# Kernel optimization log

Hardware: AMD Instinct MI355X
Metric: run time of the kernel (lower is better)

## Reference

```python
import jax, jax.numpy as jnp
import numpy as np

B, T, C, H = 8, 4096, 1024, 64

def setup_inputs() -> dict:
    key = jax.random.key(0)
    k1, k2, k3, k4 = jax.random.split(key, 4)
    return {
        "x": jax.random.normal(k1, (B, T, C), dtype=jnp.float32),
        "Wq": jax.random.normal(k2, (C, H), dtype=jnp.float32) * (C ** -0.5),
        "Wk": jax.random.normal(k3, (C, H), dtype=jnp.float32) * (C ** -0.5),
        "Wv": jax.random.normal(k4, (C, H), dtype=jnp.float32) * (C ** -0.5),
    }

def reference(x, Wq, Wk, Wv):
    # x: [B, T, C]; projections are bias-free Linears
    q = jnp.einsum("btc,ch->bth", x, Wq)  # [B, T, H]
    k = jnp.einsum("btc,ch->bth", x, Wk)
    v = jnp.einsum("btc,ch->bth", x, Wv)
    # NOTE: original scales by C**-0.5 (embed size), not head_size**-0.5
    scores = jnp.einsum("bqh,bkh->bqk", q, k) * (x.shape[-1] ** -0.5)  # [B, T, T]
    causal = jnp.tril(jnp.ones((x.shape[1], x.shape[1]), dtype=bool))
    scores = jnp.where(causal, scores, -jnp.inf)
    weights = jax.nn.softmax(scores, axis=-1)
    # dropout p=0.0 (eval) -> identity
    return jnp.einsum("bqk,bkh->bqh", weights, v)  # [B, T, H]
```

## Files before the change

kernel.cpp:

```cpp
#include <hip/hip_runtime.h>
#include <hip/hip_bf16.h>

typedef __attribute__((ext_vector_type(8))) short short8;
typedef __attribute__((ext_vector_type(4))) float f32x4;
typedef unsigned short u16;
typedef unsigned int u32;
typedef unsigned long long u64;

typedef u64    __attribute__((may_alias)) u64a;
typedef short8 __attribute__((may_alias)) short8a;
typedef float4 __attribute__((may_alias)) float4a;

#define Tseq 4096
#define LPP  72

__device__ __forceinline__ u32 pk_bf(float a, float b) {
    union { __hip_bfloat162 h; u32 u; } t;
    float2 f; f.x = a; f.y = b;
    t.h = __float22bfloat162_rn(f);
    return t.u;
}

__device__ __forceinline__ u16 f2bf(float f) {
    u32 u = __float_as_uint(f);
    u = (u + 0x7FFFu + ((u >> 16) & 1u)) >> 16;
    return (u16)u;
}

__device__ __forceinline__ short8 ld_frag_lds(const u16* p) {
    union { short8 v; u64 u[2]; } t;
    t.u[0] = *(const u64a*)(p);
    t.u[1] = *(const u64a*)(p + 4);
    return t.v;
}

__device__ __forceinline__ short8 cvt8(float4 a, float4 b) {
    union { short8 s; u32 u[4]; } t;
    t.u[0] = pk_bf(a.x, a.y); t.u[1] = pk_bf(a.z, a.w);
    t.u[2] = pk_bf(b.x, b.y); t.u[3] = pk_bf(b.z, b.w);
    return t.s;
}

__device__ __forceinline__ void gld_lds16(const void* g, void* l) {
    __builtin_amdgcn_global_load_lds(
        (const __attribute__((address_space(1))) u32*)g,
        (__attribute__((address_space(3))) u32*)l, 16, 0, 0);
}

__global__ __launch_bounds__(256) void wt_kernel(const float* __restrict__ Wq,
                                                 const float* __restrict__ Wk,
                                                 const float* __restrict__ Wv,
                                                 u16* __restrict__ wtf) {
    int idx = blockIdx.x * 256 + threadIdx.x;
    int lane = idx & 63, cc = (idx >> 6) & 31, n = (idx >> 11) & 3, mat = idx >> 13;
    const float* W = (mat == 0) ? Wq : ((mat == 1) ? Wk : Wv);
    float sc = (mat == 0) ? 0.03125f : 1.0f;
    int h = n * 16 + (lane & 15);
    int cbase = cc * 32 + (lane >> 4) * 8;
    union { short8 s; u32 u[4]; } t;
#pragma unroll
    for (int j2 = 0; j2 < 4; ++j2) {
        float a = W[(size_t)(cbase + j2 * 2)     * 64 + h] * sc;
        float b = W[(size_t)(cbase + j2 * 2 + 1) * 64 + h] * sc;
        t.u[j2] = pk_bf(a, b);
    }
    *(short8a*)(wtf + (size_t)idx * 8) = t.s;
}

__global__ __launch_bounds__(256, 2) void proj_kernel(const float* __restrict__ x,
                                                      const u16* __restrict__ wtf,
                                                      u16* __restrict__ qb,
                                                      u16* __restrict__ kA,
                                                      u16* __restrict__ vA) {
    __shared__ __align__(16) u16 Wl[2][12 * 2 * 64 * 8];

    const int tid = threadIdx.x, lane = tid & 63, wave = tid >> 6;
    const int m = lane & 15, quad = lane >> 4;
    const long rowbase = (long)blockIdx.x * 64 + wave * 16;
    const float* xr = x + (rowbase + m) * 1024 + quad * 8;

    f32x4 acc[12];
#pragma unroll
    for (int i = 0; i < 12; ++i) acc[i] = (f32x4){0.f, 0.f, 0.f, 0.f};

#define STAGE(p, buf)                                                          \
    {                                                                          \
        _Pragma("unroll")                                                      \
        for (int i = 0; i < 6; ++i) {                                          \
            int c = wave * 6 + i, mn = c >> 1, ccp = c & 1;                    \
            const u16* g = wtf + ((size_t)(mn * 32 + (p) * 2 + ccp) * 64 + lane) * 8; \
            u16* l = &Wl[buf][(size_t)(mn * 2 + ccp) * 512];                   \
            gld_lds16(g, l);                                                   \
        }                                                                      \
    }

    float4 xa[4], xb[4];
#pragma unroll
    for (int t = 0; t < 4; ++t)
        xa[t] = *(const float4a*)(xr + (t >> 1) * 32 + (t & 1) * 4);
#pragma unroll
    for (int t = 0; t < 4; ++t)
        xb[t] = *(const float4a*)(xr + (2 + (t >> 1)) * 32 + (t & 1) * 4);

    STAGE(0, 0);
    __syncthreads();

    for (int p = 0; p < 16; ++p) {
        if (p < 15) STAGE(p + 1, (p + 1) & 1);
        float4 xn[4];
        if (p < 14) {
#pragma unroll
            for (int t = 0; t < 4; ++t)
                xn[t] = *(const float4a*)(xr + (2 * (p + 2) + (t >> 1)) * 32 + (t & 1) * 4);
        }
        const u16* wb = Wl[p & 1];
#pragma unroll
        for (int ccp = 0; ccp < 2; ++ccp) {
            short8 af = cvt8(xa[ccp * 2], xa[ccp * 2 + 1]);
#pragma unroll
            for (int mn = 0; mn < 12; ++mn) {
                short8 bf = *(const short8a*)(wb + ((size_t)(mn * 2 + ccp) * 64 + lane) * 8);
                acc[mn] = __builtin_amdgcn_mfma_f32_16x16x32_bf16(af, bf, acc[mn], 0, 0, 0);
            }
        }
#pragma unroll
        for (int t = 0; t < 4; ++t) { xa[t] = xb[t]; if (p < 14) xb[t] = xn[t]; }
        __syncthreads();
    }
#undef STAGE

    const int b  = (int)(rowbase >> 12);
    const int tb = (int)(rowbase & 4095);

#pragma unroll
    for (int n = 0; n < 4; ++n)
#pragma unroll
        for (int r = 0; r < 4; ++r)
            qb[(rowbase + quad * 4 + r) * 64 + n * 16 + m] = f2bf(acc[n][r]);

#pragma unroll
    for (int n = 0; n < 4; ++n) {
        int kk = n >> 1;
        int lq = (n * 2 + (m >> 3)) & 3;
        int j  = m & 7;
#pragma unroll
        for (int r = 0; r < 4; ++r) {
            int key = tb + quad * 4 + r;
            size_t a = ((((size_t)b * 256 + (key >> 4)) * 2 + kk) * 64
                        + ((key & 15) + 16 * lq)) * 8 + j;
            kA[a] = f2bf(acc[4 + n][r]);
        }
    }

    {
        int key0 = tb + quad * 4;
        int j0 = key0 & 7;
        int q2 = (key0 >> 3) & 3;
        int kc = key0 >> 5;
#pragma unroll
        for (int n = 0; n < 4; ++n) {
            u64 pv = (u64)pk_bf(acc[8 + n][0], acc[8 + n][1])
                   | ((u64)pk_bf(acc[8 + n][2], acc[8 + n][3]) << 32);
            size_t a = ((((size_t)b * 4 + n) * 128 + kc) * 64 + (m + 16 * q2)) * 8 + j0;
            *(u64a*)(vA + a) = pv;
        }
    }
}

struct K8 { short8 k[8]; };

__device__ __forceinline__ void loadK(K8& f, const u16* kAb, int kt, int lane) {
    const u16* kp = kAb + (size_t)kt * 4096 + (size_t)lane * 8;
#pragma unroll
    for (int mt = 0; mt < 4; ++mt) {
        f.k[mt * 2]     = *(const short8a*)(kp + mt * 1024);
        f.k[mt * 2 + 1] = *(const short8a*)(kp + mt * 1024 + 512);
    }
}

__device__ __forceinline__ void attn_step(const K8& f, const u16* vAb,
        short8 qf0, short8 qf1, u16* pw,
        f32x4& o0, f32x4& o1, f32x4& o2, f32x4& o3,
        float& lsum, int kt, int n_s, int qrow, int quad, int m, int lane) {
    const float L2E = 1.4426950408889634f;
    const float FMB = 4.0f * L2E;
    const u16* vp = vAb + (size_t)kt * 1024 + (size_t)lane * 8;
    short8 vf[8];
#pragma unroll
    for (int ht = 0; ht < 4; ++ht) {
        vf[ht * 2]     = *(const short8a*)(vp + (size_t)ht * 65536);
        vf[ht * 2 + 1] = *(const short8a*)(vp + (size_t)ht * 65536 + 512);
    }
    f32x4 s[4];
#pragma unroll
    for (int mt = 0; mt < 4; ++mt) {
        f32x4 a = (f32x4){0.f, 0.f, 0.f, 0.f};
        a = __builtin_amdgcn_mfma_f32_16x16x32_bf16(f.k[mt * 2],     qf0, a, 0, 0, 0);
        a = __builtin_amdgcn_mfma_f32_16x16x32_bf16(f.k[mt * 2 + 1], qf1, a, 0, 0, 0);
        s[mt] = a;
    }
    if (kt == n_s) {
#pragma unroll
        for (int mt = 0; mt < 4; ++mt)
#pragma unroll
            for (int r = 0; r < 4; ++r) {
                int key = kt * 64 + mt * 16 + quad * 4 + r;
                if (key > qrow) s[mt][r] = -1e30f;
            }
    }
#pragma unroll
    for (int mt = 0; mt < 4; ++mt) {
        float p0 = __builtin_amdgcn_exp2f(s[mt][0] * L2E - FMB);
        float p1 = __builtin_amdgcn_exp2f(s[mt][1] * L2E - FMB);
        float p2 = __builtin_amdgcn_exp2f(s[mt][2] * L2E - FMB);
        float p3 = __builtin_amdgcn_exp2f(s[mt][3] * L2E - FMB);
        lsum += (p0 + p1) + (p2 + p3);
        u64 pv = (u64)pk_bf(p0, p1) | ((u64)pk_bf(p2, p3) << 32);
        *(u64a*)(pw + m * LPP + mt * 16 + quad * 4) = pv;
    }
    __builtin_amdgcn_wave_barrier();
    short8 pf0 = ld_frag_lds(pw + m * LPP + quad * 8);
    short8 pf1 = ld_frag_lds(pw + m * LPP + 32 + quad * 8);
    o0 = __builtin_amdgcn_mfma_f32_16x16x32_bf16(vf[0], pf0, o0, 0, 0, 0);
    o0 = __builtin_amdgcn_mfma_f32_16x16x32_bf16(vf[1], pf1, o0, 0, 0, 0);
    o1 = __builtin_amdgcn_mfma_f32_16x16x32_bf16(vf[2], pf0, o1, 0, 0, 0);
    o1 = __builtin_amdgcn_mfma_f32_16x16x32_bf16(vf[3], pf1, o1, 0, 0, 0);
    o2 = __builtin_amdgcn_mfma_f32_16x16x32_bf16(vf[4], pf0, o2, 0, 0, 0);
    o2 = __builtin_amdgcn_mfma_f32_16x16x32_bf16(vf[5], pf1, o2, 0, 0, 0);
    o3 = __builtin_amdgcn_mfma_f32_16x16x32_bf16(vf[6], pf0, o3, 0, 0, 0);
    o3 = __builtin_amdgcn_mfma_f32_16x16x32_bf16(vf[7], pf1, o3, 0, 0, 0);
}

__global__ __launch_bounds__(256, 3) void attn_kernel(const u16* __restrict__ qb,
                                                      const u16* __restrict__ kA,
                                                      const u16* __restrict__ vA,
                                                      float* __restrict__ out) {
    __shared__ __align__(16) u16 Pt[4][16 * LPP];
    __shared__ float Ob[2][16][64];
    __shared__ float Lb[2][64];

    const int tid = threadIdx.x, lane = tid & 63, wave = tid >> 6;
    const int m = lane & 15, quad = lane >> 4;
    const int beta = blockIdx.x;
    const int b = beta & 7, u = beta >> 3;
    const int role = (wave + beta) & 3;
    const int slot = role >> 1;
    const int half = role & 1;
    const int s = slot ? (255 - u) : u;
    const int qbase = s * 16;
    const int n_s = s >> 2;
    const int h = (n_s + 1) >> 1;
    const int kt0 = half ? h : 0;
    const int kt1 = half ? n_s : (h - 1);

    const u16* qp = qb + ((size_t)b * Tseq + qbase + m) * 64;
    short8 qf0 = *(const short8a*)(qp + quad * 8);
    short8 qf1 = *(const short8a*)(qp + 32 + quad * 8);

    const u16* kAb = kA + (size_t)b * (256 * 2 * 64 * 8);
    const u16* vAb = vA + (size_t)b * (4 * 128 * 64 * 8);
    u16* pw = Pt[wave];

    f32x4 o0 = {0.f, 0.f, 0.f, 0.f}, o1 = o0, o2 = o0, o3 = o0;
    float lsum = 0.f;
    const int qrow = qbase + m;

    if (kt0 <= kt1) {
        K8 ka, kb2;
        loadK(ka, kAb, kt0, lane);
        int kt = kt0;
        while (true) {
            if (kt < kt1) loadK(kb2, kAb, kt + 1, lane);
            attn_step(ka, vAb, qf0, qf1, pw, o0, o1, o2, o3, lsum,
                      kt, n_s, qrow, quad, m, lane);
            if (kt == kt1) break;
            ++kt;
            if (kt < kt1) loadK(ka, kAb, kt + 1, lane);
            attn_step(kb2, vAb, qf0, qf1, pw, o0, o1, o2, o3, lsum,
                      kt, n_s, qrow, quad, m, lane);
            if (kt == kt1) break;
            ++kt;
        }
    }

    if (half == 1) {
#pragma unroll
        for (int hn = 0; hn < 4; ++hn) {
            Ob[slot][hn * 4 + 0][lane] = o0[hn];
        }
        Ob[slot][0][lane] = o0[0]; Ob[slot][1][lane] = o0[1];
        Ob[slot][2][lane] = o0[2]; Ob[slot][3][lane] = o0[3];
        Ob[slot][4][lane] = o1[0]; Ob[slot][5][lane] = o1[1];
        Ob[slot][6][lane] = o1[2]; Ob[slot][7][lane] = o1[3];
        Ob[slot][8][lane] = o2[0]; Ob[slot][9][lane] = o2[1];
        Ob[slot][10][lane] = o2[2]; Ob[slot][11][lane] = o2[3];
        Ob[slot][12][lane] = o3[0]; Ob[slot][13][lane] = o3[1];
        Ob[slot][14][lane] = o3[2]; Ob[slot][15][lane] = o3[3];
        Lb[slot][lane] = lsum;
    }
    __syncthreads();
    if (half == 0) {
        o0[0] += Ob[slot][0][lane]; o0[1] += Ob[slot][1][lane];
        o0[2] += Ob[slot][2][lane]; o0[3] += Ob[slot][3][lane];
        o1[0] += Ob[slot][4][lane]; o1[1] += Ob[slot][5][lane];
        o1[2] += Ob[slot][6][lane]; o1[3] += Ob[slot][7][lane];
        o2[0] += Ob[slot][8][lane]; o2[1] += Ob[slot][9][lane];
        o2[2] += Ob[slot][10][lane]; o2[3] += Ob[slot][11][lane];
        o3[0] += Ob[slot][12][lane]; o3[1] += Ob[slot][13][lane];
        o3[2] += Ob[slot][14][lane]; o3[3] += Ob[slot][15][lane];
        lsum += Lb[slot][lane];

        lsum += __shfl_xor(lsum, 16, 64);
        lsum += __shfl_xor(lsum, 32, 64);
        float inv = 1.0f / lsum;

        float* orow = out + ((size_t)b * Tseq + qbase + m) * 64;
        float4 w;
        w.x = o0[0] * inv; w.y = o0[1] * inv; w.z = o0[2] * inv; w.w = o0[3] * inv;
        *(float4a*)(orow + 0 * 16 + quad * 4) = w;
        w.x = o1[0] * inv; w.y = o1[1] * inv; w.z = o1[2] * inv; w.w = o1[3] * inv;
        *(float4a*)(orow + 1 * 16 + quad * 4) = w;
        w.x = o2[0] * inv; w.y = o2[1] * inv; w.z = o2[2] * inv; w.w = o2[3] * inv;
        *(float4a*)(orow + 2 * 16 + quad * 4) = w;
        w.x = o3[0] * inv; w.y = o3[1] * inv; w.z = o3[2] * inv; w.w = o3[3] * inv;
        *(float4a*)(orow + 3 * 16 + quad * 4) = w;
    }
}

extern "C" void kernel_launch(void* const* d_in, const int* in_sizes, int n_in,
                              void* d_out, int out_size, void* d_ws, size_t ws_size,
                              hipStream_t stream) {
    const float* x  = (const float*)d_in[0];
    const float* Wq = (const float*)d_in[1];
    const float* Wk = (const float*)d_in[2];
    const float* Wv = (const float*)d_in[3];
    float* out = (float*)d_out;

    char* ws = (char*)d_ws;
    u16* wtf = (u16*)ws;
    u16* qb  = (u16*)(ws + 512 * 1024);
    u16* kA  = (u16*)(ws + 512 * 1024 + 4 * 1024 * 1024);
    u16* vA  = (u16*)(ws + 512 * 1024 + 8 * 1024 * 1024);

    wt_kernel<<<96, 256, 0, stream>>>(Wq, Wk, Wv, wtf);
    proj_kernel<<<512, 256, 0, stream>>>(x, wtf, qb, kA, vA);
    attn_kernel<<<1024, 256, 0, stream>>>(qb, kA, vA, out);
}
```

Before: 253.2 us.

## Balance causal key-tile work across waves with adaptive 1/3 or 2/2 strip split

Each block processes a short and a long causal query strip. Before, each strip got exactly two waves splitting its key tiles in half. Now the kernel computes, per block, whether giving the short strip one wave and the long strip three waves, or two and two, gives the smaller maximum per-wave tile count. Key tiles are then partitioned evenly among that strip's waves. Partial outputs and row sums are reduced through a larger shared buffer. The aim is to cut the slowest wave's work per block, at the cost of more LDS and a short reduction loop.

```diff
diff --git a/kernel.cpp b/kernel.cpp
--- a/kernel.cpp
+++ b/kernel.cpp
@@ -236,22 +236,32 @@
                                                       const u16* __restrict__ vA,
                                                       float* __restrict__ out) {
     __shared__ __align__(16) u16 Pt[4][16 * LPP];
-    __shared__ float Ob[2][16][64];
-    __shared__ float Lb[2][64];
+    __shared__ float Ob[4][16][64];
+    __shared__ float Lb[4][64];
 
     const int tid = threadIdx.x, lane = tid & 63, wave = tid >> 6;
     const int m = lane & 15, quad = lane >> 4;
     const int beta = blockIdx.x;
     const int b = beta & 7, u = beta >> 3;
-    const int role = (wave + beta) & 3;
-    const int slot = role >> 1;
-    const int half = role & 1;
-    const int s = slot ? (255 - u) : u;
+
+    const int T0 = (u >> 2) + 1;
+    const int T1 = 64 - (u >> 2);
+    const int max13 = (T0 > (T1 + 2) / 3) ? T0 : (T1 + 2) / 3;
+    const int c22a = (T0 + 1) >> 1, c22b = (T1 + 1) >> 1;
+    const int max22 = (c22a > c22b) ? c22a : c22b;
+    const int n0 = (max13 <= max22) ? 1 : 2;
+    const int n1 = 4 - n0;
+
+    const int r = (wave + beta) & 3;
+    const int strip_id = (r < n0) ? 0 : 1;
+    const int part   = strip_id ? (r - n0) : r;
+    const int nparts = strip_id ? n1 : n0;
+    const int T      = strip_id ? T1 : T0;
+    const int s      = strip_id ? (255 - u) : u;
     const int qbase = s * 16;
     const int n_s = s >> 2;
-    const int h = (n_s + 1) >> 1;
-    const int kt0 = half ? h : 0;
-    const int kt1 = half ? n_s : (h - 1);
+    const int kt0 = part * T / nparts;
+    const int kt1 = (part + 1) * T / nparts - 1;
 
     const u16* qp = qb + ((size_t)b * Tseq + qbase + m) * 64;
     short8 qf0 = *(const short8a*)(qp + quad * 8);
@@ -283,32 +293,32 @@
         }
     }
 
-    if (half == 1) {
-#pragma unroll
-        for (int hn = 0; hn < 4; ++hn) {
-            Ob[slot][hn * 4 + 0][lane] = o0[hn];
-        }
-        Ob[slot][0][lane] = o0[0]; Ob[slot][1][lane] = o0[1];
-        Ob[slot][2][lane] = o0[2]; Ob[slot][3][lane] = o0[3];
-        Ob[slot][4][lane] = o1[0]; Ob[slot][5][lane] = o1[1];
-        Ob[slot][6][lane] = o1[2]; Ob[slot][7][lane] = o1[3];
-        Ob[slot][8][lane] = o2[0]; Ob[slot][9][lane] = o2[1];
-        Ob[slot][10][lane] = o2[2]; Ob[slot][11][lane] = o2[3];
-        Ob[slot][12][lane] = o3[0]; Ob[slot][13][lane] = o3[1];
-        Ob[slot][14][lane] = o3[2]; Ob[slot][15][lane] = o3[3];
-        Lb[slot][lane] = lsum;
+    if (part != 0) {
+        Ob[r][0][lane] = o0[0]; Ob[r][1][lane] = o0[1];
+        Ob[r][2][lane] = o0[2]; Ob[r][3][lane] = o0[3];
+        Ob[r][4][lane] = o1[0]; Ob[r][5][lane] = o1[1];
+        Ob[r][6][lane] = o1[2]; Ob[r][7][lane] = o1[3];
+        Ob[r][8][lane] = o2[0]; Ob[r][9][lane] = o2[1];
+        Ob[r][10][lane] = o2[2]; Ob[r][11][lane] = o2[3];
+        Ob[r][12][lane] = o3[0]; Ob[r][13][lane] = o3[1];
+        Ob[r][14][lane] = o3[2]; Ob[r][15][lane] = o3[3];
+        Lb[r][lane] = lsum;
     }
     __syncthreads();
-    if (half == 0) {
-        o0[0] += Ob[slot][0][lane]; o0[1] += Ob[slot][1][lane];
-        o0[2] += Ob[slot][2][lane]; o0[3] += Ob[slot][3][lane];
-        o1[0] += Ob[slot][4][lane]; o1[1] += Ob[slot][5][lane];
-        o1[2] += Ob[slot][6][lane]; o1[3] += Ob[slot][7][lane];
-        o2[0] += Ob[slot][8][lane]; o2[1] += Ob[slot][9][lane];
-        o2[2] += Ob[slot][10][lane]; o2[3] += Ob[slot][11][lane];
-        o3[0] += Ob[slot][12][lane]; o3[1] += Ob[slot][13][lane];
-        o3[2] += Ob[slot][14][lane]; o3[3] += Ob[slot][15][lane];
-        lsum += Lb[slot][lane];
+    if (part == 0) {
+#pragma unroll 1
+        for (int pr = 1; pr < nparts; ++pr) {
+            const int rr = r + pr;
+            o0[0] += Ob[rr][0][lane]; o0[1] += Ob[rr][1][lane];
+            o0[2] += Ob[rr][2][lane]; o0[3] += Ob[rr][3][lane];
+            o1[0] += Ob[rr][4][lane]; o1[1] += Ob[rr][5][lane];
+            o1[2] += Ob[rr][6][lane]; o1[3] += Ob[rr][7][lane];
+            o2[0] += Ob[rr][8][lane]; o2[1] += Ob[rr][9][lane];
+            o2[2] += Ob[rr][10][lane]; o2[3] += Ob[rr][11][lane];
+            o3[0] += Ob[rr][12][lane]; o3[1] += Ob[rr][13][lane];
+            o3[2] += Ob[rr][14][lane]; o3[3] += Ob[rr][15][lane];
+            lsum += Lb[rr][lane];
+        }
 
         lsum += __shfl_xor(lsum, 16, 64);
         lsum += __shfl_xor(lsum, 32, 64);
```

After: 252.3 us. About the same (-0.4%).

## Share K/V tiles across four query waves via double-buffered LDS staging

Applied to the files above, without the earlier changes.

The attention kernel changes from each wave streaming its own K/V fragments from global memory (with a two-wave split-KV and an LDS reduction) to each block handling 64 consecutive query rows. The four waves cooperatively load each 64-key K/V tile into double-buffered shared memory with gld_lds16, and every wave reads it from there. The aim is to cut redundant global/L2 traffic for K and V and to drop the split-KV combine step. In exchange there is a block-wide barrier per key tile, more LDS use, lower occupancy (launch bounds 2, 512 blocks), and coarser causal load balance.

```diff
diff --git a/kernel.cpp b/kernel.cpp
--- a/kernel.cpp
+++ b/kernel.cpp
@@ -167,91 +167,22 @@
     }
 }
 
-struct K8 { short8 k[8]; };
-
-__device__ __forceinline__ void loadK(K8& f, const u16* kAb, int kt, int lane) {
-    const u16* kp = kAb + (size_t)kt * 4096 + (size_t)lane * 8;
-#pragma unroll
-    for (int mt = 0; mt < 4; ++mt) {
-        f.k[mt * 2]     = *(const short8a*)(kp + mt * 1024);
-        f.k[mt * 2 + 1] = *(const short8a*)(kp + mt * 1024 + 512);
-    }
-}
-
-__device__ __forceinline__ void attn_step(const K8& f, const u16* vAb,
-        short8 qf0, short8 qf1, u16* pw,
-        f32x4& o0, f32x4& o1, f32x4& o2, f32x4& o3,
-        float& lsum, int kt, int n_s, int qrow, int quad, int m, int lane) {
-    const float L2E = 1.4426950408889634f;
-    const float FMB = 4.0f * L2E;
-    const u16* vp = vAb + (size_t)kt * 1024 + (size_t)lane * 8;
-    short8 vf[8];
-#pragma unroll
-    for (int ht = 0; ht < 4; ++ht) {
-        vf[ht * 2]     = *(const short8a*)(vp + (size_t)ht * 65536);
-        vf[ht * 2 + 1] = *(const short8a*)(vp + (size_t)ht * 65536 + 512);
-    }
-    f32x4 s[4];
-#pragma unroll
-    for (int mt = 0; mt < 4; ++mt) {
-        f32x4 a = (f32x4){0.f, 0.f, 0.f, 0.f};
-        a = __builtin_amdgcn_mfma_f32_16x16x32_bf16(f.k[mt * 2],     qf0, a, 0, 0, 0);
-        a = __builtin_amdgcn_mfma_f32_16x16x32_bf16(f.k[mt * 2 + 1], qf1, a, 0, 0, 0);
-        s[mt] = a;
-    }
-    if (kt == n_s) {
-#pragma unroll
-        for (int mt = 0; mt < 4; ++mt)
-#pragma unroll
-            for (int r = 0; r < 4; ++r) {
-                int key = kt * 64 + mt * 16 + quad * 4 + r;
-                if (key > qrow) s[mt][r] = -1e30f;
-            }
-    }
-#pragma unroll
-    for (int mt = 0; mt < 4; ++mt) {
-        float p0 = __builtin_amdgcn_exp2f(s[mt][0] * L2E - FMB);
-        float p1 = __builtin_amdgcn_exp2f(s[mt][1] * L2E - FMB);
-        float p2 = __builtin_amdgcn_exp2f(s[mt][2] * L2E - FMB);
-        float p3 = __builtin_amdgcn_exp2f(s[mt][3] * L2E - FMB);
-        lsum += (p0 + p1) + (p2 + p3);
-        u64 pv = (u64)pk_bf(p0, p1) | ((u64)pk_bf(p2, p3) << 32);
-        *(u64a*)(pw + m * LPP + mt * 16 + quad * 4) = pv;
-    }
-    __builtin_amdgcn_wave_barrier();
-    short8 pf0 = ld_frag_lds(pw + m * LPP + quad * 8);
-    short8 pf1 = ld_frag_lds(pw + m * LPP + 32 + quad * 8);
-    o0 = __builtin_amdgcn_mfma_f32_16x16x32_bf16(vf[0], pf0, o0, 0, 0, 0);
-    o0 = __builtin_amdgcn_mfma_f32_16x16x32_bf16(vf[1], pf1, o0, 0, 0, 0);
-    o1 = __builtin_amdgcn_mfma_f32_16x16x32_bf16(vf[2], pf0, o1, 0, 0, 0);
-    o1 = __builtin_amdgcn_mfma_f32_16x16x32_bf16(vf[3], pf1, o1, 0, 0, 0);
-    o2 = __builtin_amdgcn_mfma_f32_16x16x32_bf16(vf[4], pf0, o2, 0, 0, 0);
-    o2 = __builtin_amdgcn_mfma_f32_16x16x32_bf16(vf[5], pf1, o2, 0, 0, 0);
-    o3 = __builtin_amdgcn_mfma_f32_16x16x32_bf16(vf[6], pf0, o3, 0, 0, 0);
-    o3 = __builtin_amdgcn_mfma_f32_16x16x32_bf16(vf[7], pf1, o3, 0, 0, 0);
-}
-
-__global__ __launch_bounds__(256, 3) void attn_kernel(const u16* __restrict__ qb,
+__global__ __launch_bounds__(256, 2) void attn_kernel(const u16* __restrict__ qb,
                                                       const u16* __restrict__ kA,
                                                       const u16* __restrict__ vA,
                                                       float* __restrict__ out) {
+    __shared__ __align__(16) u16 KVl[2][2][4096];
     __shared__ __align__(16) u16 Pt[4][16 * LPP];
-    __shared__ float Ob[2][16][64];
-    __shared__ float Lb[2][64];
 
     const int tid = threadIdx.x, lane = tid & 63, wave = tid >> 6;
     const int m = lane & 15, quad = lane >> 4;
     const int beta = blockIdx.x;
-    const int b = beta & 7, u = beta >> 3;
-    const int role = (wave + beta) & 3;
-    const int slot = role >> 1;
-    const int half = role & 1;
-    const int s = slot ? (255 - u) : u;
-    const int qbase = s * 16;
-    const int n_s = s >> 2;
-    const int h = (n_s + 1) >> 1;
-    const int kt0 = half ? h : 0;
-    const int kt1 = half ? n_s : (h - 1);
+    const int b = beta & 7;
+    const int u = beta >> 3;
+    const int g = (u < 32) ? (63 - u) : (u - 32);
+
+    const int qbase = (g * 4 + wave) * 16;
+    const int qrow = qbase + m;
 
     const u16* qp = qb + ((size_t)b * Tseq + qbase + m) * 64;
     short8 qf0 = *(const short8a*)(qp + quad * 8);
@@ -263,68 +194,109 @@
 
     f32x4 o0 = {0.f, 0.f, 0.f, 0.f}, o1 = o0, o2 = o0, o3 = o0;
     float lsum = 0.f;
-    const int qrow = qbase + m;
-
-    if (kt0 <= kt1) {
-        K8 ka, kb2;
-        loadK(ka, kAb, kt0, lane);
-        int kt = kt0;
-        while (true) {
-            if (kt < kt1) loadK(kb2, kAb, kt + 1, lane);
-            attn_step(ka, vAb, qf0, qf1, pw, o0, o1, o2, o3, lsum,
-                      kt, n_s, qrow, quad, m, lane);
-            if (kt == kt1) break;
-            ++kt;
-            if (kt < kt1) loadK(ka, kAb, kt + 1, lane);
-            attn_step(kb2, vAb, qf0, qf1, pw, o0, o1, o2, o3, lsum,
-                      kt, n_s, qrow, quad, m, lane);
-            if (kt == kt1) break;
-            ++kt;
-        }
-    }
-
-    if (half == 1) {
-#pragma unroll
-        for (int hn = 0; hn < 4; ++hn) {
-            Ob[slot][hn * 4 + 0][lane] = o0[hn];
-        }
-        Ob[slot][0][lane] = o0[0]; Ob[slot][1][lane] = o0[1];
-        Ob[slot][2][lane] = o0[2]; Ob[slot][3][lane] = o0[3];
-        Ob[slot][4][lane] = o1[0]; Ob[slot][5][lane] = o1[1];
-        Ob[slot][6][lane] = o1[2]; Ob[slot][7][lane] = o1[3];
-        Ob[slot][8][lane] = o2[0]; Ob[slot][9][lane] = o2[1];
-        Ob[slot][10][lane] = o2[2]; Ob[slot][11][lane] = o2[3];
-        Ob[slot][12][lane] = o3[0]; Ob[slot][13][lane] = o3[1];
-        Ob[slot][14][lane] = o3[2]; Ob[slot][15][lane] = o3[3];
-        Lb[slot][lane] = lsum;
-    }
+
+    const float L2E = 1.4426950408889634f;
+    const float FMB = 4.0f * L2E;
+
+#define ASTAGE(kt, bf)                                                         \
+    {                                                                          \
+        if (wave < 2) {                                                        \
+            _Pragma("unroll")                                                  \
+            for (int i = 0; i < 4; ++i) {                                      \
+                int c = wave * 4 + i;                                          \
+                const u16* gp = kAb + (size_t)(kt) * 4096 + c * 512 + lane * 8;\
+                gld_lds16(gp, &KVl[bf][0][c * 512]);                           \
+            }                                                                  \
+        } else {                                                               \
+            _Pragma("unroll")                                                  \
+            for (int i = 0; i < 4; ++i) {                                      \
+                int j = (wave - 2) * 4 + i, ht = j >> 1, hf = j & 1;           \
+                const u16* gp = vAb + (size_t)(kt) * 1024 + (size_t)ht * 65536 \
+                                + hf * 512 + lane * 8;                         \
+                gld_lds16(gp, &KVl[bf][1][ht * 1024 + hf * 512]);              \
+            }                                                                  \
+        }                                                                      \
+    }
+
+    ASTAGE(0, 0);
     __syncthreads();
-    if (half == 0) {
-        o0[0] += Ob[slot][0][lane]; o0[1] += Ob[slot][1][lane];
-        o0[2] += Ob[slot][2][lane]; o0[3] += Ob[slot][3][lane];
-        o1[0] += Ob[slot][4][lane]; o1[1] += Ob[slot][5][lane];
-        o1[2] += Ob[slot][6][lane]; o1[3] += Ob[slot][7][lane];
-        o2[0] += Ob[slot][8][lane]; o2[1] += Ob[slot][9][lane];
-        o2[2] += Ob[slot][10][lane]; o2[3] += Ob[slot][11][lane];
-        o3[0] += Ob[slot][12][lane]; o3[1] += Ob[slot][13][lane];
-        o3[2] += Ob[slot][14][lane]; o3[3] += Ob[slot][15][lane];
-        lsum += Lb[slot][lane];
-
-        lsum += __shfl_xor(lsum, 16, 64);
-        lsum += __shfl_xor(lsum, 32, 64);
-        float inv = 1.0f / lsum;
-
-        float* orow = out + ((size_t)b * Tseq + qbase + m) * 64;
-        float4 w;
-        w.x = o0[0] * inv; w.y = o0[1] * inv; w.z = o0[2] * inv; w.w = o0[3] * inv;
-        *(float4a*)(orow + 0 * 16 + quad * 4) = w;
-        w.x = o1[0] * inv; w.y = o1[1] * inv; w.z = o1[2] * inv; w.w = o1[3] * inv;
-        *(float4a*)(orow + 1 * 16 + quad * 4) = w;
-        w.x = o2[0] * inv; w.y = o2[1] * inv; w.z = o2[2] * inv; w.w = o2[3] * inv;
-        *(float4a*)(orow + 2 * 16 + quad * 4) = w;
-        w.x = o3[0] * inv; w.y = o3[1] * inv; w.z = o3[2] * inv; w.w = o3[3] * inv;
-        *(float4a*)(orow + 3 * 16 + quad * 4) = w;
-    }
+
+    int buf = 0;
+    for (int kt = 0; kt <= g; ++kt) {
+        if (kt < g) ASTAGE(kt + 1, buf ^ 1);
+
+        const u16* Klb = KVl[buf][0];
+        const u16* Vlb = KVl[buf][1];
+
+        short8 vf[8];
+#pragma unroll
+        for (int ht = 0; ht < 4; ++ht) {
+            vf[ht * 2]     = *(const short8a*)(Vlb + ht * 1024 + lane * 8);
+            vf[ht * 2 + 1] = *(const short8a*)(Vlb + ht * 1024 + 512 + lane * 8);
+        }
+
+        f32x4 s[4];
+#pragma unroll
+        for (int mt = 0; mt < 4; ++mt) {
+            short8 kf0 = *(const short8a*)(Klb + mt * 1024 + lane * 8);
+            short8 kf1 = *(const short8a*)(Klb + mt * 1024 + 512 + lane * 8);
+            f32x4 a = (f32x4){0.f, 0.f, 0.f, 0.f};
+            a = __builtin_amdgcn_mfma_f32_16x16x32_bf16(kf0, qf0, a, 0, 0, 0);
+            a = __builtin_amdgcn_mfma_f32_16x16x32_bf16(kf1, qf1, a, 0, 0, 0);
+            s[mt] = a;
+        }
+
+        if (kt == g) {
+#pragma unroll
+            for (int mt = 0; mt < 4; ++mt)
+#pragma unroll
+                for (int r = 0; r < 4; ++r) {
+                    int key = kt * 64 + mt * 16 + quad * 4 + r;
+                    if (key > qrow) s[mt][r] = -1e30f;
+                }
+        }
+
+#pragma unroll
+        for (int mt = 0; mt < 4; ++mt) {
+            float p0 = __builtin_amdgcn_exp2f(s[mt][0] * L2E - FMB);
+            float p1 = __builtin_amdgcn_exp2f(s[mt][1] * L2E - FMB);
+            float p2 = __builtin_amdgcn_exp2f(s[mt][2] * L2E - FMB);
+            float p3 = __builtin_amdgcn_exp2f(s[mt][3] * L2E - FMB);
+            lsum += (p0 + p1) + (p2 + p3);
+            u64 pv = (u64)pk_bf(p0, p1) | ((u64)pk_bf(p2, p3) << 32);
+            *(u64a*)(pw + m * LPP + mt * 16 + quad * 4) = pv;
+        }
+        __builtin_amdgcn_wave_barrier();
+        short8 pf0 = ld_frag_lds(pw + m * LPP + quad * 8);
+        short8 pf1 = ld_frag_lds(pw + m * LPP + 32 + quad * 8);
+        o0 = __builtin_amdgcn_mfma_f32_16x16x32_bf16(vf[0], pf0, o0, 0, 0, 0);
+        o0 = __builtin_amdgcn_mfma_f32_16x16x32_bf16(vf[1], pf1, o0, 0, 0, 0);
+        o1 = __builtin_amdgcn_mfma_f32_16x16x32_bf16(vf[2], pf0, o1, 0, 0, 0);
+        o1 = __builtin_amdgcn_mfma_f32_16x16x32_bf16(vf[3], pf1, o1, 0, 0, 0);
+        o2 = __builtin_amdgcn_mfma_f32_16x16x32_bf16(vf[4], pf0, o2, 0, 0, 0);
+        o2 = __builtin_amdgcn_mfma_f32_16x16x32_bf16(vf[5], pf1, o2, 0, 0, 0);
+        o3 = __builtin_amdgcn_mfma_f32_16x16x32_bf16(vf[6], pf0, o3, 0, 0, 0);
+        o3 = __builtin_amdgcn_mfma_f32_16x16x32_bf16(vf[7], pf1, o3, 0, 0, 0);
+
+        __syncthreads();
+        buf ^= 1;
+    }
+#undef ASTAGE
+
+    lsum += __shfl_xor(lsum, 16, 64);
+    lsum += __shfl_xor(lsum, 32, 64);
+    float inv = 1.0f / lsum;
+
+    float* orow = out + ((size_t)b * Tseq + qbase + m) * 64;
+    float4 w;
+    w.x = o0[0] * inv; w.y = o0[1] * inv; w.z = o0[2] * inv; w.w = o0[3] * inv;
+    *(float4a*)(orow + 0 * 16 + quad * 4) = w;
+    w.x = o1[0] * inv; w.y = o1[1] * inv; w.z = o1[2] * inv; w.w = o1[3] * inv;
+    *(float4a*)(orow + 1 * 16 + quad * 4) = w;
+    w.x = o2[0] * inv; w.y = o2[1] * inv; w.z = o2[2] * inv; w.w = o2[3] * inv;
+    *(float4a*)(orow + 2 * 16 + quad * 4) = w;
+    w.x = o3[0] * inv; w.y = o3[1] * inv; w.z = o3[2] * inv; w.w = o3[3] * inv;
+    *(float4a*)(orow + 3 * 16 + quad * 4) = w;
 }
 
 extern "C" void kernel_launch(void* const* d_in, const int* in_sizes, int n_in,
@@ -344,5 +316,5 @@
 
     wt_kernel<<<96, 256, 0, stream>>>(Wq, Wk, Wv, wtf);
     proj_kernel<<<512, 256, 0, stream>>>(x, wtf, qb, kA, vA);
-    attn_kernel<<<1024, 256, 0, stream>>>(qb, kA, vA, out);
-}
+    attn_kernel<<<512, 256, 0, stream>>>(qb, kA, vA, out);
+}
```

Measured after the change: 266.9 us. +5.4%, slower.

## Share K/V tiles across four query sub-tiles per wave with split-K reduction

Applied to the files above, without the earlier changes.

Each block now handles a 64-row query tile per batch. Each of its four waves processes a quarter of the key range for all four 16-row sub-tiles, so every loaded K/V fragment feeds four query sub-tiles instead of one. Partial outputs and row sums are published through shared memory and reduced so that each wave finalizes one sub-tile. It also adds s_setprio around the MFMA sections, halves the grid to 512 blocks and lowers launch bounds to 2 blocks per CU. The aim is to cut global/L2 traffic for K/V, at the cost of more registers (16 accumulators), a larger LDS footprint and lower occupancy.

```diff
diff --git a/kernel.cpp b/kernel.cpp
--- a/kernel.cpp
+++ b/kernel.cpp
@@ -178,20 +178,22 @@
     }
 }
 
-__device__ __forceinline__ void attn_step(const K8& f, const u16* vAb,
-        short8 qf0, short8 qf1, u16* pw,
-        f32x4& o0, f32x4& o1, f32x4& o2, f32x4& o3,
-        float& lsum, int kt, int n_s, int qrow, int quad, int m, int lane) {
-    const float L2E = 1.4426950408889634f;
-    const float FMB = 4.0f * L2E;
+__device__ __forceinline__ void loadV(short8* vf, const u16* vAb, int kt, int lane) {
     const u16* vp = vAb + (size_t)kt * 1024 + (size_t)lane * 8;
-    short8 vf[8];
 #pragma unroll
     for (int ht = 0; ht < 4; ++ht) {
         vf[ht * 2]     = *(const short8a*)(vp + (size_t)ht * 65536);
         vf[ht * 2 + 1] = *(const short8a*)(vp + (size_t)ht * 65536 + 512);
     }
+}
+
+__device__ __forceinline__ void sub_step(const K8& f, const short8* vf,
+        short8 qf0, short8 qf1, u16* pw,
+        f32x4 (&o)[4], float& lsum, int kt, int n_s, int qrow, int quad, int m) {
+    const float L2E = 1.4426950408889634f;
+    const float FMB = 4.0f * L2E;
     f32x4 s[4];
+    __builtin_amdgcn_s_setprio(1);
 #pragma unroll
     for (int mt = 0; mt < 4; ++mt) {
         f32x4 a = (f32x4){0.f, 0.f, 0.f, 0.f};
@@ -199,6 +201,7 @@
         a = __builtin_amdgcn_mfma_f32_16x16x32_bf16(f.k[mt * 2 + 1], qf1, a, 0, 0, 0);
         s[mt] = a;
     }
+    __builtin_amdgcn_s_setprio(0);
     if (kt == n_s) {
 #pragma unroll
         for (int mt = 0; mt < 4; ++mt)
@@ -221,109 +224,136 @@
     __builtin_amdgcn_wave_barrier();
     short8 pf0 = ld_frag_lds(pw + m * LPP + quad * 8);
     short8 pf1 = ld_frag_lds(pw + m * LPP + 32 + quad * 8);
-    o0 = __builtin_amdgcn_mfma_f32_16x16x32_bf16(vf[0], pf0, o0, 0, 0, 0);
-    o0 = __builtin_amdgcn_mfma_f32_16x16x32_bf16(vf[1], pf1, o0, 0, 0, 0);
-    o1 = __builtin_amdgcn_mfma_f32_16x16x32_bf16(vf[2], pf0, o1, 0, 0, 0);
-    o1 = __builtin_amdgcn_mfma_f32_16x16x32_bf16(vf[3], pf1, o1, 0, 0, 0);
-    o2 = __builtin_amdgcn_mfma_f32_16x16x32_bf16(vf[4], pf0, o2, 0, 0, 0);
-    o2 = __builtin_amdgcn_mfma_f32_16x16x32_bf16(vf[5], pf1, o2, 0, 0, 0);
-    o3 = __builtin_amdgcn_mfma_f32_16x16x32_bf16(vf[6], pf0, o3, 0, 0, 0);
-    o3 = __builtin_amdgcn_mfma_f32_16x16x32_bf16(vf[7], pf1, o3, 0, 0, 0);
-}
-
-__global__ __launch_bounds__(256, 3) void attn_kernel(const u16* __restrict__ qb,
+    __builtin_amdgcn_s_setprio(1);
+    o[0] = __builtin_amdgcn_mfma_f32_16x16x32_bf16(vf[0], pf0, o[0], 0, 0, 0);
+    o[0] = __builtin_amdgcn_mfma_f32_16x16x32_bf16(vf[1], pf1, o[0], 0, 0, 0);
+    o[1] = __builtin_amdgcn_mfma_f32_16x16x32_bf16(vf[2], pf0, o[1], 0, 0, 0);
+    o[1] = __builtin_amdgcn_mfma_f32_16x16x32_bf16(vf[3], pf1, o[1], 0, 0, 0);
+    o[2] = __builtin_amdgcn_mfma_f32_16x16x32_bf16(vf[4], pf0, o[2], 0, 0, 0);
+    o[2] = __builtin_amdgcn_mfma_f32_16x16x32_bf16(vf[5], pf1, o[2], 0, 0, 0);
+    o[3] = __builtin_amdgcn_mfma_f32_16x16x32_bf16(vf[6], pf0, o[3], 0, 0, 0);
+    o[3] = __builtin_amdgcn_mfma_f32_16x16x32_bf16(vf[7], pf1, o[3], 0, 0, 0);
+    __builtin_amdgcn_s_setprio(0);
+}
+
+__global__ __launch_bounds__(256, 2) void attn_kernel(const u16* __restrict__ qb,
                                                       const u16* __restrict__ kA,
                                                       const u16* __restrict__ vA,
                                                       float* __restrict__ out) {
-    __shared__ __align__(16) u16 Pt[4][16 * LPP];
-    __shared__ float Ob[2][16][64];
-    __shared__ float Lb[2][64];
+    __shared__ __align__(16) u16 Pt[4][2][16 * LPP];
+    __shared__ float Pub[4][3][16][64];
+    __shared__ float Lpub[4][3][64];
 
     const int tid = threadIdx.x, lane = tid & 63, wave = tid >> 6;
     const int m = lane & 15, quad = lane >> 4;
     const int beta = blockIdx.x;
-    const int b = beta & 7, u = beta >> 3;
-    const int role = (wave + beta) & 3;
-    const int slot = role >> 1;
-    const int half = role & 1;
-    const int s = slot ? (255 - u) : u;
-    const int qbase = s * 16;
-    const int n_s = s >> 2;
-    const int h = (n_s + 1) >> 1;
-    const int kt0 = half ? h : 0;
-    const int kt1 = half ? n_s : (h - 1);
-
-    const u16* qp = qb + ((size_t)b * Tseq + qbase + m) * 64;
-    short8 qf0 = *(const short8a*)(qp + quad * 8);
-    short8 qf1 = *(const short8a*)(qp + 32 + quad * 8);
+    const int b = beta & 7;
+    const int u = beta >> 3;
+    const int g = (u < 32) ? (63 - u) : (u - 32);
+    const int T = g + 1;
+
+    const int kt0 = wave * T / 4;
+    const int kt1 = (wave + 1) * T / 4 - 1;
+
+    const int qbase = g * 64;
+
+    short8 qf[4][2];
+#pragma unroll
+    for (int ss = 0; ss < 4; ++ss) {
+        const u16* qp = qb + ((size_t)b * Tseq + qbase + ss * 16 + m) * 64;
+        qf[ss][0] = *(const short8a*)(qp + quad * 8);
+        qf[ss][1] = *(const short8a*)(qp + 32 + quad * 8);
+    }
 
     const u16* kAb = kA + (size_t)b * (256 * 2 * 64 * 8);
     const u16* vAb = vA + (size_t)b * (4 * 128 * 64 * 8);
-    u16* pw = Pt[wave];
-
-    f32x4 o0 = {0.f, 0.f, 0.f, 0.f}, o1 = o0, o2 = o0, o3 = o0;
-    float lsum = 0.f;
-    const int qrow = qbase + m;
+
+    f32x4 o[4][4];
+#pragma unroll
+    for (int ss = 0; ss < 4; ++ss)
+#pragma unroll
+        for (int ht = 0; ht < 4; ++ht) o[ss][ht] = (f32x4){0.f, 0.f, 0.f, 0.f};
+    float ls[4] = {0.f, 0.f, 0.f, 0.f};
+
+#define QSTEP(KF)                                                              \
+    {                                                                          \
+        _Pragma("unroll")                                                      \
+        for (int ss = 0; ss < 4; ++ss)                                         \
+            sub_step(KF, vf, qf[ss][0], qf[ss][1], Pt[wave][ss & 1],           \
+                     o[ss], ls[ss], kt, g, qbase + ss * 16 + m, quad, m);      \
+    }
 
     if (kt0 <= kt1) {
         K8 ka, kb2;
+        short8 vf[8];
         loadK(ka, kAb, kt0, lane);
         int kt = kt0;
         while (true) {
+            loadV(vf, vAb, kt, lane);
             if (kt < kt1) loadK(kb2, kAb, kt + 1, lane);
-            attn_step(ka, vAb, qf0, qf1, pw, o0, o1, o2, o3, lsum,
-                      kt, n_s, qrow, quad, m, lane);
+            QSTEP(ka);
             if (kt == kt1) break;
             ++kt;
+            loadV(vf, vAb, kt, lane);
             if (kt < kt1) loadK(ka, kAb, kt + 1, lane);
-            attn_step(kb2, vAb, qf0, qf1, pw, o0, o1, o2, o3, lsum,
-                      kt, n_s, qrow, quad, m, lane);
+            QSTEP(kb2);
             if (kt == kt1) break;
             ++kt;
         }
     }
-
-    if (half == 1) {
-#pragma unroll
-        for (int hn = 0; hn < 4; ++hn) {
-            Ob[slot][hn * 4 + 0][lane] = o0[hn];
-        }
-        Ob[slot][0][lane] = o0[0]; Ob[slot][1][lane] = o0[1];
-        Ob[slot][2][lane] = o0[2]; Ob[slot][3][lane] = o0[3];
-        Ob[slot][4][lane] = o1[0]; Ob[slot][5][lane] = o1[1];
-        Ob[slot][6][lane] = o1[2]; Ob[slot][7][lane] = o1[3];
-        Ob[slot][8][lane] = o2[0]; Ob[slot][9][lane] = o2[1];
-        Ob[slot][10][lane] = o2[2]; Ob[slot][11][lane] = o2[3];
-        Ob[slot][12][lane] = o3[0]; Ob[slot][13][lane] = o3[1];
-        Ob[slot][14][lane] = o3[2]; Ob[slot][15][lane] = o3[3];
-        Lb[slot][lane] = lsum;
+#undef QSTEP
+
+#pragma unroll
+    for (int ss = 0; ss < 4; ++ss) {
+        if (ss != wave) {
+            const int k = ss - (ss > wave ? 1 : 0);
+#pragma unroll
+            for (int ht = 0; ht < 4; ++ht) {
+                Pub[wave][k][ht * 4 + 0][lane] = o[ss][ht][0];
+                Pub[wave][k][ht * 4 + 1][lane] = o[ss][ht][1];
+                Pub[wave][k][ht * 4 + 2][lane] = o[ss][ht][2];
+                Pub[wave][k][ht * 4 + 3][lane] = o[ss][ht][3];
+            }
+            Lpub[wave][k][lane] = ls[ss];
+        }
     }
     __syncthreads();
-    if (half == 0) {
-        o0[0] += Ob[slot][0][lane]; o0[1] += Ob[slot][1][lane];
-        o0[2] += Ob[slot][2][lane]; o0[3] += Ob[slot][3][lane];
-        o1[0] += Ob[slot][4][lane]; o1[1] += Ob[slot][5][lane];
-        o1[2] += Ob[slot][6][lane]; o1[3] += Ob[slot][7][lane];
-        o2[0] += Ob[slot][8][lane]; o2[1] += Ob[slot][9][lane];
-        o2[2] += Ob[slot][10][lane]; o2[3] += Ob[slot][11][lane];
-        o3[0] += Ob[slot][12][lane]; o3[1] += Ob[slot][13][lane];
-        o3[2] += Ob[slot][14][lane]; o3[3] += Ob[slot][15][lane];
-        lsum += Lb[slot][lane];
-
-        lsum += __shfl_xor(lsum, 16, 64);
-        lsum += __shfl_xor(lsum, 32, 64);
-        float inv = 1.0f / lsum;
-
-        float* orow = out + ((size_t)b * Tseq + qbase + m) * 64;
-        float4 w;
-        w.x = o0[0] * inv; w.y = o0[1] * inv; w.z = o0[2] * inv; w.w = o0[3] * inv;
-        *(float4a*)(orow + 0 * 16 + quad * 4) = w;
-        w.x = o1[0] * inv; w.y = o1[1] * inv; w.z = o1[2] * inv; w.w = o1[3] * inv;
-        *(float4a*)(orow + 1 * 16 + quad * 4) = w;
-        w.x = o2[0] * inv; w.y = o2[1] * inv; w.z = o2[2] * inv; w.w = o2[3] * inv;
-        *(float4a*)(orow + 2 * 16 + quad * 4) = w;
-        w.x = o3[0] * inv; w.y = o3[1] * inv; w.z = o3[2] * inv; w.w = o3[3] * inv;
-        *(float4a*)(orow + 3 * 16 + quad * 4) = w;
+
+    f32x4 mo[4];
+    float mls = 0.f;
+#pragma unroll
+    for (int ss = 0; ss < 4; ++ss)
+        if (ss == wave) {
+            mo[0] = o[ss][0]; mo[1] = o[ss][1];
+            mo[2] = o[ss][2]; mo[3] = o[ss][3];
+            mls = ls[ss];
+        }
+
+#pragma unroll 1
+    for (int w = 0; w < 4; ++w) {
+        if (w == wave) continue;
+        const int k = wave - (wave > w ? 1 : 0);
+#pragma unroll
+        for (int ht = 0; ht < 4; ++ht) {
+            mo[ht][0] += Pub[w][k][ht * 4 + 0][lane];
+            mo[ht][1] += Pub[w][k][ht * 4 + 1][lane];
+            mo[ht][2] += Pub[w][k][ht * 4 + 2][lane];
+            mo[ht][3] += Pub[w][k][ht * 4 + 3][lane];
+        }
+        mls += Lpub[w][k][lane];
+    }
+
+    mls += __shfl_xor(mls, 16, 64);
+    mls += __shfl_xor(mls, 32, 64);
+    float inv = 1.0f / mls;
+
+    float* orow = out + ((size_t)b * Tseq + qbase + wave * 16 + m) * 64;
+    float4 wv;
+#pragma unroll
+    for (int ht = 0; ht < 4; ++ht) {
+        wv.x = mo[ht][0] * inv; wv.y = mo[ht][1] * inv;
+        wv.z = mo[ht][2] * inv; wv.w = mo[ht][3] * inv;
+        *(float4a*)(orow + ht * 16 + quad * 4) = wv;
     }
 }
 
@@ -344,5 +374,5 @@
 
     wt_kernel<<<96, 256, 0, stream>>>(Wq, Wk, Wv, wtf);
     proj_kernel<<<512, 256, 0, stream>>>(x, wtf, qb, kA, vA);
-    attn_kernel<<<1024, 256, 0, stream>>>(qb, kA, vA, out);
-}
+    attn_kernel<<<512, 256, 0, stream>>>(qb, kA, vA, out);
+}
```

Measured after the change: 314.1 us. 1.24x slower.
